# Performance work log

Measured on AMD Instinct MI355X. Metric: run time of the kernel, lower is better.

Reference implementation:

```python
import jax, jax.numpy as jnp
import numpy as np

IMAGE_SIZE = 224          # config.image_size
RP_Q = 10 / 100.0         # config.rp_percentage, 'point' threshold mode
EPS = 1e-8                # normalize_minmax eps
CLIP = 1e-6               # arccos clamp margin


def minmax_global(x):
    """normalize_minmax over the whole tensor (as applied to the raw series)."""
    lo, hi = x.min(), x.max()
    rng = hi - lo
    return jnp.where(rng < EPS, jnp.zeros_like(x), (x - lo) / (rng + EPS))


def minmax_per_matrix(x):
    """normalize_minmax applied independently per (b, d) LxL matrix."""
    lo = x.min(axis=(-2, -1), keepdims=True)
    hi = x.max(axis=(-2, -1), keepdims=True)
    rng = hi - lo
    return jnp.where(rng < EPS, jnp.zeros_like(x), (x - lo) / (rng + EPS))


def setup_inputs() -> dict:
    key = jax.random.key(0)
    x = jax.random.normal(key, (4, 1024, 8), dtype=jnp.float32)  # [B, L, D]
    return {"x": x}


def reference(x):
    B, L, D = x.shape

    # ---- Gramian Angular Field (summation), vectorized over (b, d) ----
    x_norm = minmax_global(x) * 2.0 - 1.0                       # [B, L, D]
    theta = jnp.arccos(jnp.clip(x_norm, -1.0 + CLIP, 1.0 - CLIP))
    th = jnp.transpose(theta, (0, 2, 1))                        # [B, D, L]
    gaf = jnp.cos(th[:, :, :, None] + th[:, :, None, :])        # [B, D, L, L]
    gaf = minmax_per_matrix(gaf)

    # ---- Recurrence plot ('point' quantile threshold), vectorized ----
    s = jnp.transpose(x, (0, 2, 1))                             # [B, D, L]
    dist = jnp.abs(s[:, :, :, None] - s[:, :, None, :])         # [B, D, L, L]
    thr = jnp.quantile(dist.reshape(B, D, L * L), RP_Q, axis=-1)
    rp = (dist <= thr[:, :, None, None]).astype(x.dtype)        # [B, D, L, L]

    # ---- Bilinear resize to (image_size, image_size), align_corners=False ----
    out = jnp.concatenate([gaf, rp], axis=1)                    # [B, 2D, L, L]
    out = jax.image.resize(out, (B, 2 * D, IMAGE_SIZE, IMAGE_SIZE),
                           method="bilinear", antialias=False)
    return out
```

## Files before the change

### kernel.cpp

```cpp
#include <hip/hip_runtime.h>
#include <cfloat>
#include <math.h>

#define B_ 4
#define L_ 1024
#define D_ 8
#define OUT_ 224
#define NPIX (B_ * 2 * D_ * OUT_ * OUT_)
#define NT4  (NPIX / 4)
#define TBL 128
#define TSTR 896

#define NPLANE 32
#define PB 16
#define NBLK (NPLANE * PB)
#define NBIN 2048
#define SLOTCAP 1024
#define GCAP 8192
#define R1U 51917u
#define R2U 51918u

#define SC_PHIST 0u
#define SC_PGAF  ((unsigned)NBLK * (unsigned)NBIN)
#define SC_CNT   (SC_PGAF + (unsigned)NBLK * 2u)
#define SC_BRK   (SC_CNT + (unsigned)NBLK)
#define SC_SLOT  (SC_BRK + (unsigned)NPLANE * 4u)

__device__ __forceinline__ float clipnorm(float v, float lo, float inv2, int degen) {
    float xn = degen ? -1.0f : ((v - lo) * inv2 - 1.0f);
    return fminf(fmaxf(xn, -1.0f + 1e-6f), 1.0f - 1e-6f);
}

__device__ __forceinline__ float sort64(float val, int tid) {
#pragma unroll
    for (int k = 2; k <= 64; k <<= 1) {
        bool up = ((tid & k) == 0);
#pragma unroll
        for (int j = k >> 1; j > 0; j >>= 1) {
            float o = __shfl_xor(val, j);
            bool lower = ((tid & j) == 0);
            float mn = fminf(val, o), mx = fmaxf(val, o);
            val = (lower == up) ? mn : mx;
        }
    }
    return val;
}

__global__ __launch_bounds__(1024) void k_minmax(const float* __restrict__ x,
                                                 float* __restrict__ ws) {
    __shared__ float red[32];
    const int tid  = threadIdx.x;
    const int lane = tid & 63;
    const int wave = tid >> 6;

    float lo = FLT_MAX, hi = -FLT_MAX;
    const float4* x4 = (const float4*)x;
    for (int i = tid; i < (B_ * L_ * D_) / 4; i += 1024) {
        float4 q = x4[i];
        lo = fminf(fminf(fminf(lo, q.x), q.y), fminf(q.z, q.w));
        hi = fmaxf(fmaxf(fmaxf(hi, q.x), q.y), fmaxf(q.z, q.w));
    }
#pragma unroll
    for (int off = 32; off; off >>= 1) {
        lo = fminf(lo, __shfl_down(lo, off));
        hi = fmaxf(hi, __shfl_down(hi, off));
    }
    if (lane == 0) { red[wave] = lo; red[16 + wave] = hi; }
    __syncthreads();
    if (wave == 0 && lane < 16) {
        float l2 = red[lane], h2 = red[16 + lane];
#pragma unroll
        for (int off = 8; off; off >>= 1) {
            l2 = fminf(l2, __shfl_down(l2, off));
            h2 = fmaxf(h2, __shfl_down(h2, off));
        }
        if (lane == 0) { ws[0] = l2; ws[1] = h2; }
    }
}

__global__ __launch_bounds__(256) void k_pairs(const float* __restrict__ x,
                                               const float* __restrict__ ws,
                                               float* __restrict__ wsw,
                                               unsigned* __restrict__ scratch) {
    __shared__ __align__(16) float4 S4[L_];
    __shared__ unsigned hist[NBIN];
    __shared__ float red[16];

    const int tid  = threadIdx.x;
    const int lane = tid & 63;
    const int wave = tid >> 6;
    const int bid  = blockIdx.x;
    const int p    = bid >> 4;
    const int bip  = bid & 15;
    const int b    = p >> 3, d = p & 7;

    const float glo = ws[0], ghi = ws[1];
    const float rng   = ghi - glo;
    const int   degen = rng < 1e-8f;
    const float inv2  = 2.0f / (rng + 1e-8f);
    const float scale = (float)(NBIN - 1) / fmaxf(rng, 1e-20f);

    for (int i = tid; i < L_; i += 256) {
        float v = x[(b * L_ + i) * D_ + d];
        float c = clipnorm(v, glo, inv2, degen);
        S4[i] = make_float4(v, c, sqrtf(fmaxf(0.0f, 1.0f - c * c)), 0.0f);
    }
    for (int i = tid; i < NBIN; i += 256) hist[i] = 0u;
    __syncthreads();

    float4 col[4];
#pragma unroll
    for (int q = 0; q < 4; q++) col[q] = S4[tid + q * 256];

    float gmn = FLT_MAX, gmx = -FLT_MAX;
#pragma unroll
    for (int q = 0; q < 4; q++) {
        float g = col[q].y * col[q].y - col[q].z * col[q].z;
        gmn = fminf(gmn, g); gmx = fmaxf(gmx, g);
    }

    const int obase = bip * 32;
    for (int oo = 1; oo <= 32; ++oo) {
        const int o = obase + oo;
        const int nq = (o == 512) ? 2 : 4;
#pragma unroll
        for (int q = 0; q < 4; q++) {
            if (q < nq) {
                int jp = (tid + q * 256 + o) & 1023;
                float4 P = S4[jp];
                float dd = fabsf(col[q].x - P.x);
                int bin = min((int)(dd * scale), NBIN - 1);
                atomicAdd(&hist[bin], 1u);
                float g = col[q].y * P.y - col[q].z * P.z;
                gmn = fminf(gmn, g); gmx = fmaxf(gmx, g);
            }
        }
    }
    __syncthreads();

    {
        unsigned* ph = scratch + SC_PHIST + (unsigned)bid * NBIN;
        for (int i = tid; i < NBIN; i += 256) ph[i] = hist[i];
    }
#pragma unroll
    for (int off = 32; off; off >>= 1) {
        gmn = fminf(gmn, __shfl_down(gmn, off));
        gmx = fmaxf(gmx, __shfl_down(gmx, off));
    }
    if (lane == 0) { red[wave] = gmn; red[8 + wave] = gmx; }
    __syncthreads();
    if (tid == 0) {
        float* pg = (float*)scratch + SC_PGAF + bid * 2;
        pg[0] = fminf(fminf(red[0], red[1]), fminf(red[2], red[3]));
        pg[1] = fmaxf(fmaxf(red[8], red[9]), fmaxf(red[10], red[11]));
    }
    if (bip == 0) {
        const float scL = (float)L_ / (float)OUT_;
        float* basep = wsw + TBL + p * TSTR;
        for (int o = tid; o < OUT_; o += 256) {
            float fx = (o + 0.5f) * scL - 0.5f;
            int x0 = (int)fx; float wx = fx - (float)x0;
            float q0 = x[(b * L_ + x0) * D_ + d];
            float q1 = x[(b * L_ + x0 + 1) * D_ + d];
            float c0 = clipnorm(q0, glo, inv2, degen), c1 = clipnorm(q1, glo, inv2, degen);
            float s0 = sqrtf(fmaxf(0.0f, 1.0f - c0 * c0)), s1 = sqrtf(fmaxf(0.0f, 1.0f - c1 * c1));
            basep[o]        = c0 + wx * (c1 - c0);
            basep[OUT_ + o] = s0 + wx * (s1 - s0);
            basep[448 + o]  = q0;
            basep[672 + o]  = q1;
        }
    }
}

__global__ __launch_bounds__(256) void k_bracket(float* __restrict__ ws,
                                                 unsigned* __restrict__ scratch) {
    __shared__ unsigned wsum[4];
    __shared__ unsigned sB1, sB2, sBase;

    const int tid  = threadIdx.x;
    const int lane = tid & 63;
    const int wave = tid >> 6;
    const int p    = blockIdx.x;

    unsigned loc[8];
#pragma unroll
    for (int q = 0; q < 8; q++) loc[q] = 0u;
    const unsigned* ph = scratch + SC_PHIST + (unsigned)(p * PB) * NBIN;
    for (int k = 0; k < PB; k++) {
        const uint4* ph4 = (const uint4*)(ph + (unsigned)k * NBIN) + tid * 2;
        uint4 a = ph4[0], c4 = ph4[1];
        loc[0] += a.x; loc[1] += a.y; loc[2] += a.z; loc[3] += a.w;
        loc[4] += c4.x; loc[5] += c4.y; loc[6] += c4.z; loc[7] += c4.w;
    }
    unsigned tsum = 0u;
#pragma unroll
    for (int q = 0; q < 8; q++) tsum += loc[q];
    unsigned inc = tsum;
#pragma unroll
    for (int off = 1; off < 64; off <<= 1) {
        unsigned o = __shfl_up(inc, off);
        if (lane >= off) inc += o;
    }
    if (lane == 63) wsum[wave] = inc;
    __syncthreads();
    unsigned woff = 0u;
    for (int w2 = 0; w2 < 4; w2++) woff += (w2 < wave) ? wsum[w2] : 0u;
    unsigned run = woff + inc - tsum;
#pragma unroll
    for (int q = 0; q < 8; q++) {
        unsigned prev = run; run += loc[q];
        if (prev < R1U && run >= R1U) { sB1 = (unsigned)(tid * 8 + q); sBase = prev; }
        if (prev < R2U && run >= R2U) { sB2 = (unsigned)(tid * 8 + q); }
    }
    __syncthreads();
    if (tid == 0) {
        unsigned* brk = scratch + SC_BRK + (unsigned)p * 4u;
        brk[0] = sB1; brk[1] = sB2; brk[2] = sBase;
    }
    if (tid < 16) {
        const float* pg = (const float*)scratch + SC_PGAF + (unsigned)(p * PB + tid) * 2u;
        float mn = pg[0], mx = pg[1];
#pragma unroll
        for (int off = 8; off; off >>= 1) {
            mn = fminf(mn, __shfl_down(mn, off));
            mx = fmaxf(mx, __shfl_down(mx, off));
        }
        if (tid == 0) {
            ws[2 + p * 3 + 0] = mn;
            ws[2 + p * 3 + 1] = mx;
        }
    }
}

__global__ __launch_bounds__(256) void k_collect(const float* __restrict__ x,
                                                 const float* __restrict__ ws,
                                                 unsigned* __restrict__ scratch) {
    __shared__ float s[L_];
    __shared__ float stage[SLOTCAP];
    __shared__ unsigned scnt;

    const int tid  = threadIdx.x;
    const int bid  = blockIdx.x;
    const int p    = bid >> 4;
    const int bip  = bid & 15;
    const int b    = p >> 3, d = p & 7;

    const float glo = ws[0], ghi = ws[1];
    const float scale = (float)(NBIN - 1) / fmaxf(ghi - glo, 1e-20f);

    const unsigned* brk = scratch + SC_BRK + (unsigned)p * 4u;
    const unsigned B1 = brk[0], B2 = brk[1];
    const float fB1   = (float)B1;
    const float fB2p1 = (B2 >= (unsigned)(NBIN - 1)) ? FLT_MAX : (float)(B2 + 1u);

    for (int i = tid; i < L_; i += 256) s[i] = x[(b * L_ + i) * D_ + d];
    if (tid == 0) scnt = 0u;
    __syncthreads();

    float sj[4];
#pragma unroll
    for (int q = 0; q < 4; q++) sj[q] = s[tid + q * 256];

    const int obase = bip * 32;
    for (int oo = 1; oo <= 32; ++oo) {
        const int o = obase + oo;
        const int nq = (o == 512) ? 2 : 4;
#pragma unroll
        for (int q = 0; q < 4; q++) {
            if (q < nq) {
                int jp = (tid + q * 256 + o) & 1023;
                float dd = fabsf(sj[q] - s[jp]);
                float y = dd * scale;
                if (y >= fB1 && y < fB2p1) {
                    unsigned idx = atomicAdd(&scnt, 1u);
                    if (idx < (unsigned)SLOTCAP) stage[idx] = dd;
                }
            }
        }
    }
    __syncthreads();
    {
        unsigned bc = scnt; bc = (bc < (unsigned)SLOTCAP) ? bc : (unsigned)SLOTCAP;
        float* slot = (float*)scratch + SC_SLOT + (unsigned)bid * SLOTCAP;
        for (unsigned idx = tid; idx < bc; idx += 256) slot[idx] = stage[idx];
        if (tid == 0) scratch[SC_CNT + bid] = bc;
    }
}

__global__ __launch_bounds__(256) void k_select(float* __restrict__ ws,
                                                const unsigned* __restrict__ scratch) {
    __shared__ float cand[GCAP];
    __shared__ float nbuf[2048];
    __shared__ unsigned h2[1024];
    __shared__ unsigned wsum[4];
    __shared__ unsigned scnt, sT1, sT2, sC1, sH1, uminb, umaxb;
    __shared__ float sv1, sv2;
    __shared__ unsigned cpre[17];

    const int tid  = threadIdx.x;
    const int lane = tid & 63;
    const int wave = tid >> 6;
    const int p    = blockIdx.x;

    const float glo = ws[0], ghi = ws[1];
    const float scale = (float)(NBIN - 1) / fmaxf(ghi - glo, 1e-20f);

    const unsigned* brk = scratch + SC_BRK + (unsigned)p * 4u;
    const unsigned B1 = brk[0], B2 = brk[1], base = brk[2];

    if (wave == 0) {
        unsigned c = (lane < PB) ? scratch[SC_CNT + (unsigned)(p * PB + lane)] : 0u;
        unsigned incc = c;
#pragma unroll
        for (int off = 1; off < 16; off <<= 1) {
            unsigned o = __shfl_up(incc, off);
            if ((lane & 15) >= off) incc += o;
        }
        if (lane < PB) { cpre[lane] = incc - c; if (lane == PB - 1) cpre[16] = incc; }
    }
    __syncthreads();

    unsigned n = cpre[16]; n = (n < (unsigned)GCAP) ? n : (unsigned)GCAP;
    for (int k = 0; k < PB; k++) {
        unsigned off = cpre[k];
        unsigned ck  = ((k + 1 < PB) ? cpre[k + 1] : cpre[16]) - cpre[k];
        const float* slot = (const float*)scratch + SC_SLOT + (unsigned)(p * PB + k) * SLOTCAP;
        for (unsigned idx = tid; idx < ck; idx += 256) {
            unsigned dst = off + idx;
            if (dst < (unsigned)GCAP) cand[dst] = slot[idx];
        }
    }
    __syncthreads();

    float* cur = cand;
    float* nxt = nbuf;
    unsigned ncur = n;
    unsigned r1 = R1U - base;
    float vlo = (float)B1 / scale;
    float vhi = (float)(B2 + 1u) / scale;
    float v1 = 0.0f, v2 = 0.0f;
    bool done = false;

    for (int it = 0; it < 6 && !done; ++it) {
        if (tid == 0) scnt = 0u;
#pragma unroll
        for (int q = 0; q < 4; q++) h2[tid + q * 256] = 0u;
        __syncthreads();

        if (ncur <= 64u) {
            if (tid < 64) {
                float val = ((unsigned)tid < ncur) ? cur[tid] : FLT_MAX;
                val = sort64(val, tid);
                float v1l = __shfl(val, (int)r1 - 1);
                float v2l = __shfl(val, (int)r1);
                if (tid == 0) { sv1 = v1l; sv2 = v2l; }
            }
            __syncthreads();
            v1 = sv1; v2 = sv2;
            done = true;
            break;
        }

        float sc2 = 1023.0f / fmaxf(vhi - vlo, 1e-30f);
        for (unsigned k = tid; k < ncur; k += 256) {
            int bb = (int)((cur[k] - vlo) * sc2);
            bb = max(0, min(bb, 1023));
            atomicAdd(&h2[bb], 1u);
        }
        __syncthreads();

        unsigned l[4];
#pragma unroll
        for (int q = 0; q < 4; q++) l[q] = h2[4 * tid + q];
        unsigned tsum = l[0] + l[1] + l[2] + l[3];
        unsigned inc = tsum;
#pragma unroll
        for (int off = 1; off < 64; off <<= 1) {
            unsigned o = __shfl_up(inc, off);
            if (lane >= off) inc += o;
        }
        if (lane == 63) wsum[wave] = inc;
        __syncthreads();
        unsigned woff = 0u;
        for (int w2 = 0; w2 < 4; w2++) woff += (w2 < wave) ? wsum[w2] : 0u;
        unsigned prev = woff + inc - tsum;
#pragma unroll
        for (int q = 0; q < 4; q++) {
            unsigned nrun = prev + l[q];
            if (prev < r1 && nrun >= r1) { sT1 = 4u * tid + q; sC1 = prev; sH1 = l[q]; }
            if (prev < r1 + 1u && nrun >= r1 + 1u) { sT2 = 4u * tid + q; }
            prev = nrun;
        }
        __syncthreads();
        const unsigned t1 = sT1, t2 = sT2, c1 = sC1, h1 = sH1;

        if (t1 != t2) {
            if (tid == 0) { uminb = 0xFFFFFFFFu; umaxb = 0u; }
            __syncthreads();
            for (unsigned k = tid; k < ncur; k += 256) {
                float val = cur[k];
                int bb = (int)((val - vlo) * sc2);
                bb = max(0, min(bb, 1023));
                if (bb == (int)t1) atomicMax(&umaxb, __float_as_uint(val));
                else if (bb > (int)t1) atomicMin(&uminb, __float_as_uint(val));
            }
            __syncthreads();
            v1 = __uint_as_float(umaxb);
            v2 = __uint_as_float(uminb);
            done = true;
            break;
        }

        if (h1 <= 64u) {
            for (unsigned k = tid; k < ncur; k += 256) {
                float val = cur[k];
                int bb = (int)((val - vlo) * sc2);
                bb = max(0, min(bb, 1023));
                if (bb == (int)t1) {
                    unsigned idx = atomicAdd(&scnt, 1u);
                    if (idx < 64u) nxt[idx] = val;
                }
            }
            __syncthreads();
            unsigned cnt = (scnt < 64u) ? scnt : 64u;
            unsigned rr = r1 - c1;
            if (tid < 64) {
                float val = ((unsigned)tid < cnt) ? nxt[tid] : FLT_MAX;
                val = sort64(val, tid);
                float v1l = __shfl(val, (int)rr - 1);
                float v2l = __shfl(val, (int)rr);
                if (tid == 0) { sv1 = v1l; sv2 = v2l; }
            }
            __syncthreads();
            v1 = sv1; v2 = sv2;
            done = true;
            break;
        }

        for (unsigned k = tid; k < ncur; k += 256) {
            float val = cur[k];
            int bb = (int)((val - vlo) * sc2);
            bb = max(0, min(bb, 1023));
            if (bb == (int)t1) {
                unsigned idx = atomicAdd(&scnt, 1u);
                if (idx < 2048u) nxt[idx] = val;
            }
        }
        __syncthreads();
        ncur = (scnt < 2048u) ? scnt : 2048u;
        r1 = r1 - c1;
        float nvlo = vlo + (float)t1 / sc2;
        float nvhi = vlo + (float)(t1 + 1u) / sc2;
        vlo = nvlo; vhi = nvhi;
        float* tmp = cur; cur = nxt; nxt = tmp;
        __syncthreads();
    }
    if (!done) { v1 = vlo; v2 = vhi; }

    if (tid == 0) ws[2 + p * 3 + 2] = v1 + (v2 - v1) * 0.5f;
}

__global__ __launch_bounds__(256) void k_out(const float* __restrict__ ws,
                                             float4* __restrict__ out4) {
    __shared__ __align__(16) float lds[448];
    __shared__ float sc[3];

    const int tid = threadIdx.x;
    int plane = blockIdx.x / 49;
    int c = plane & 15, b = plane >> 4, d = c & 7;

    const float* tb = ws + TBL + (b * 8 + d) * TSTR + ((c < 8) ? 0 : 448);
    for (int i = tid; i < 448; i += 256) lds[i] = tb[i];
    if (tid == 0) {
        if (c < 8) {
            float mn = ws[2 + (b * 8 + d) * 3 + 0];
            float mx = ws[2 + (b * 8 + d) * 3 + 1];
            float g = mx - mn;
            sc[0] = mn;
            sc[1] = (g < 1e-8f) ? 0.0f : 1.0f / (g + 1e-8f);
            sc[2] = (g < 1e-8f) ? 1.0f : 0.0f;
        } else {
            sc[0] = ws[2 + (b * 8 + d) * 3 + 2];
        }
    }
    __syncthreads();

    int tix = blockIdx.x * 256 + tid;
    int pix0 = tix << 2;
    int ox0 = pix0 % OUT_;
    int oy  = (pix0 / OUT_) % OUT_;

    float4 r;
    if (c < 8) {
        float mn = sc[0], ginv = sc[1];
        bool gdeg = sc[2] != 0.0f;
        float Cr = lds[oy], Sr = lds[OUT_ + oy];
        float4 Cc = *(const float4*)&lds[ox0];
        float4 Sc = *(const float4*)&lds[OUT_ + ox0];
        r.x = gdeg ? 0.0f : ((Cr * Cc.x - Sr * Sc.x) - mn) * ginv;
        r.y = gdeg ? 0.0f : ((Cr * Cc.y - Sr * Sc.y) - mn) * ginv;
        r.z = gdeg ? 0.0f : ((Cr * Cc.z - Sr * Sc.z) - mn) * ginv;
        r.w = gdeg ? 0.0f : ((Cr * Cc.w - Sr * Sc.w) - mn) * ginv;
    } else {
        float thr = sc[0];
        const float scale = (float)L_ / (float)OUT_;
        float fy = (oy + 0.5f) * scale - 0.5f;
        int y0 = (int)fy; float wy = fy - (float)y0;
        float r0 = lds[oy], r1 = lds[OUT_ + oy];
        float4 q0 = *(const float4*)&lds[ox0];
        float4 q1 = *(const float4*)&lds[OUT_ + ox0];
        float qq0[4] = {q0.x, q0.y, q0.z, q0.w};
        float qq1[4] = {q1.x, q1.y, q1.z, q1.w};
        float res[4];
#pragma unroll
        for (int pq = 0; pq < 4; pq++) {
            float fx = (ox0 + pq + 0.5f) * scale - 0.5f;
            int x0i = (int)fx; float wx = fx - (float)x0i;
            float v00 = (fabsf(r0 - qq0[pq]) <= thr) ? 1.0f : 0.0f;
            float v01 = (fabsf(r0 - qq1[pq]) <= thr) ? 1.0f : 0.0f;
            float v10 = (fabsf(r1 - qq0[pq]) <= thr) ? 1.0f : 0.0f;
            float v11 = (fabsf(r1 - qq1[pq]) <= thr) ? 1.0f : 0.0f;
            float top = v00 + wx * (v01 - v00);
            float bot = v10 + wx * (v11 - v10);
            res[pq] = top + wy * (bot - top);
        }
        r = make_float4(res[0], res[1], res[2], res[3]);
    }
    out4[tix] = r;
}

extern "C" void kernel_launch(void* const* d_in, const int* in_sizes, int n_in,
                              void* d_out, int out_size, void* d_ws, size_t ws_size,
                              hipStream_t stream) {
    const float* x = (const float*)d_in[0];
    float* ws = (float*)d_ws;
    unsigned* scratch = (unsigned*)d_out;

    k_minmax<<<1, 1024, 0, stream>>>(x, ws);
    k_pairs<<<NBLK, 256, 0, stream>>>(x, ws, ws, scratch);
    k_bracket<<<NPLANE, 256, 0, stream>>>(ws, scratch);
    k_collect<<<NBLK, 256, 0, stream>>>(x, ws, scratch);
    k_select<<<NPLANE, 256, 0, stream>>>(ws, scratch);
    k_out<<<NT4 / 256, 256, 0, stream>>>(ws, (float4*)d_out);
}
```

Measured before the change: 115.9 us.

## Fold global minmax and bracket search into pair and collect kernels

Removes the separate single-block minmax kernel: every k_pairs block now recomputes the global min/max of x itself, and block 0 writes it to the workspace. Removes the k_bracket kernel: every k_collect block redoes the histogram prefix scan for its plane, and only the first block of each plane writes the bracket and GAF min/max out. Splits the shared histogram into four per-wave copies to cut atomic contention, then sums them on write-out. This saves two launches and their serialization gaps, at the cost of redundant reads of x and the per-plane histograms in every block, plus four times the shared memory for histograms.

```diff
diff --git a/kernel.cpp b/kernel.cpp
--- a/kernel.cpp
+++ b/kernel.cpp
@@ -46,44 +46,11 @@
     return val;
 }
 
-__global__ __launch_bounds__(1024) void k_minmax(const float* __restrict__ x,
-                                                 float* __restrict__ ws) {
-    __shared__ float red[32];
-    const int tid  = threadIdx.x;
-    const int lane = tid & 63;
-    const int wave = tid >> 6;
-
-    float lo = FLT_MAX, hi = -FLT_MAX;
-    const float4* x4 = (const float4*)x;
-    for (int i = tid; i < (B_ * L_ * D_) / 4; i += 1024) {
-        float4 q = x4[i];
-        lo = fminf(fminf(fminf(lo, q.x), q.y), fminf(q.z, q.w));
-        hi = fmaxf(fmaxf(fmaxf(hi, q.x), q.y), fmaxf(q.z, q.w));
-    }
-#pragma unroll
-    for (int off = 32; off; off >>= 1) {
-        lo = fminf(lo, __shfl_down(lo, off));
-        hi = fmaxf(hi, __shfl_down(hi, off));
-    }
-    if (lane == 0) { red[wave] = lo; red[16 + wave] = hi; }
-    __syncthreads();
-    if (wave == 0 && lane < 16) {
-        float l2 = red[lane], h2 = red[16 + lane];
-#pragma unroll
-        for (int off = 8; off; off >>= 1) {
-            l2 = fminf(l2, __shfl_down(l2, off));
-            h2 = fmaxf(h2, __shfl_down(h2, off));
-        }
-        if (lane == 0) { ws[0] = l2; ws[1] = h2; }
-    }
-}
-
 __global__ __launch_bounds__(256) void k_pairs(const float* __restrict__ x,
-                                               const float* __restrict__ ws,
-                                               float* __restrict__ wsw,
+                                               float* __restrict__ ws,
                                                unsigned* __restrict__ scratch) {
     __shared__ __align__(16) float4 S4[L_];
-    __shared__ unsigned hist[NBIN];
+    __shared__ __align__(16) unsigned HIST[4 * NBIN];
     __shared__ float red[16];
 
     const int tid  = threadIdx.x;
@@ -94,18 +61,41 @@
     const int bip  = bid & 15;
     const int b    = p >> 3, d = p & 7;
 
-    const float glo = ws[0], ghi = ws[1];
+    float lo = FLT_MAX, hi = -FLT_MAX;
+    {
+        const float4* x4 = (const float4*)x;
+        for (int i = tid; i < (B_ * L_ * D_) / 4; i += 256) {
+            float4 q = x4[i];
+            lo = fminf(fminf(fminf(lo, q.x), q.y), fminf(q.z, q.w));
+            hi = fmaxf(fmaxf(fmaxf(hi, q.x), q.y), fmaxf(q.z, q.w));
+        }
+#pragma unroll
+        for (int off = 32; off; off >>= 1) {
+            lo = fminf(lo, __shfl_down(lo, off));
+            hi = fmaxf(hi, __shfl_down(hi, off));
+        }
+        if (lane == 0) { red[wave] = lo; red[8 + wave] = hi; }
+    }
+    __syncthreads();
+    const float glo = fminf(fminf(red[0], red[1]), fminf(red[2], red[3]));
+    const float ghi = fmaxf(fmaxf(red[8], red[9]), fmaxf(red[10], red[11]));
     const float rng   = ghi - glo;
     const int   degen = rng < 1e-8f;
     const float inv2  = 2.0f / (rng + 1e-8f);
     const float scale = (float)(NBIN - 1) / fmaxf(rng, 1e-20f);
 
+    if (bid == 0 && tid == 0) { ws[0] = glo; ws[1] = ghi; }
+
     for (int i = tid; i < L_; i += 256) {
         float v = x[(b * L_ + i) * D_ + d];
         float c = clipnorm(v, glo, inv2, degen);
         S4[i] = make_float4(v, c, sqrtf(fmaxf(0.0f, 1.0f - c * c)), 0.0f);
     }
-    for (int i = tid; i < NBIN; i += 256) hist[i] = 0u;
+    {
+        uint4 z = make_uint4(0u, 0u, 0u, 0u);
+        uint4* h4 = (uint4*)HIST;
+        for (int i = tid; i < NBIN; i += 256) h4[i] = z;
+    }
     __syncthreads();
 
     float4 col[4];
@@ -119,6 +109,7 @@
         gmn = fminf(gmn, g); gmx = fmaxf(gmx, g);
     }
 
+    unsigned* hw = HIST + wave * NBIN;
     const int obase = bip * 32;
     for (int oo = 1; oo <= 32; ++oo) {
         const int o = obase + oo;
@@ -130,7 +121,7 @@
                 float4 P = S4[jp];
                 float dd = fabsf(col[q].x - P.x);
                 int bin = min((int)(dd * scale), NBIN - 1);
-                atomicAdd(&hist[bin], 1u);
+                atomicAdd(&hw[bin], 1u);
                 float g = col[q].y * P.y - col[q].z * P.z;
                 gmn = fminf(gmn, g); gmx = fmaxf(gmx, g);
             }
@@ -140,7 +131,8 @@
 
     {
         unsigned* ph = scratch + SC_PHIST + (unsigned)bid * NBIN;
-        for (int i = tid; i < NBIN; i += 256) ph[i] = hist[i];
+        for (int i = tid; i < NBIN; i += 256)
+            ph[i] = HIST[i] + HIST[NBIN + i] + HIST[2 * NBIN + i] + HIST[3 * NBIN + i];
     }
 #pragma unroll
     for (int off = 32; off; off >>= 1) {
@@ -156,7 +148,7 @@
     }
     if (bip == 0) {
         const float scL = (float)L_ / (float)OUT_;
-        float* basep = wsw + TBL + p * TSTR;
+        float* basep = ws + TBL + p * TSTR;
         for (int o = tid; o < OUT_; o += 256) {
             float fx = (o + 0.5f) * scL - 0.5f;
             int x0 = (int)fx; float wx = fx - (float)x0;
@@ -172,74 +164,17 @@
     }
 }
 
-__global__ __launch_bounds__(256) void k_bracket(float* __restrict__ ws,
+__global__ __launch_bounds__(256) void k_collect(const float* __restrict__ x,
+                                                 float* __restrict__ ws,
                                                  unsigned* __restrict__ scratch) {
+    __shared__ float s[L_];
+    __shared__ float stage[SLOTCAP];
     __shared__ unsigned wsum[4];
-    __shared__ unsigned sB1, sB2, sBase;
+    __shared__ unsigned sB1, sB2, sBase, scnt;
 
     const int tid  = threadIdx.x;
     const int lane = tid & 63;
     const int wave = tid >> 6;
-    const int p    = blockIdx.x;
-
-    unsigned loc[8];
-#pragma unroll
-    for (int q = 0; q < 8; q++) loc[q] = 0u;
-    const unsigned* ph = scratch + SC_PHIST + (unsigned)(p * PB) * NBIN;
-    for (int k = 0; k < PB; k++) {
-        const uint4* ph4 = (const uint4*)(ph + (unsigned)k * NBIN) + tid * 2;
-        uint4 a = ph4[0], c4 = ph4[1];
-        loc[0] += a.x; loc[1] += a.y; loc[2] += a.z; loc[3] += a.w;
-        loc[4] += c4.x; loc[5] += c4.y; loc[6] += c4.z; loc[7] += c4.w;
-    }
-    unsigned tsum = 0u;
-#pragma unroll
-    for (int q = 0; q < 8; q++) tsum += loc[q];
-    unsigned inc = tsum;
-#pragma unroll
-    for (int off = 1; off < 64; off <<= 1) {
-        unsigned o = __shfl_up(inc, off);
-        if (lane >= off) inc += o;
-    }
-    if (lane == 63) wsum[wave] = inc;
-    __syncthreads();
-    unsigned woff = 0u;
-    for (int w2 = 0; w2 < 4; w2++) woff += (w2 < wave) ? wsum[w2] : 0u;
-    unsigned run = woff + inc - tsum;
-#pragma unroll
-    for (int q = 0; q < 8; q++) {
-        unsigned prev = run; run += loc[q];
-        if (prev < R1U && run >= R1U) { sB1 = (unsigned)(tid * 8 + q); sBase = prev; }
-        if (prev < R2U && run >= R2U) { sB2 = (unsigned)(tid * 8 + q); }
-    }
-    __syncthreads();
-    if (tid == 0) {
-        unsigned* brk = scratch + SC_BRK + (unsigned)p * 4u;
-        brk[0] = sB1; brk[1] = sB2; brk[2] = sBase;
-    }
-    if (tid < 16) {
-        const float* pg = (const float*)scratch + SC_PGAF + (unsigned)(p * PB + tid) * 2u;
-        float mn = pg[0], mx = pg[1];
-#pragma unroll
-        for (int off = 8; off; off >>= 1) {
-            mn = fminf(mn, __shfl_down(mn, off));
-            mx = fmaxf(mx, __shfl_down(mx, off));
-        }
-        if (tid == 0) {
-            ws[2 + p * 3 + 0] = mn;
-            ws[2 + p * 3 + 1] = mx;
-        }
-    }
-}
-
-__global__ __launch_bounds__(256) void k_collect(const float* __restrict__ x,
-                                                 const float* __restrict__ ws,
-                                                 unsigned* __restrict__ scratch) {
-    __shared__ float s[L_];
-    __shared__ float stage[SLOTCAP];
-    __shared__ unsigned scnt;
-
-    const int tid  = threadIdx.x;
     const int bid  = blockIdx.x;
     const int p    = bid >> 4;
     const int bip  = bid & 15;
@@ -248,14 +183,62 @@
     const float glo = ws[0], ghi = ws[1];
     const float scale = (float)(NBIN - 1) / fmaxf(ghi - glo, 1e-20f);
 
-    const unsigned* brk = scratch + SC_BRK + (unsigned)p * 4u;
-    const unsigned B1 = brk[0], B2 = brk[1];
+    for (int i = tid; i < L_; i += 256) s[i] = x[(b * L_ + i) * D_ + d];
+    if (tid == 0) scnt = 0u;
+
+    {
+        unsigned loc[8];
+#pragma unroll
+        for (int q = 0; q < 8; q++) loc[q] = 0u;
+        const unsigned* ph = scratch + SC_PHIST + (unsigned)(p * PB) * NBIN;
+        for (int k = 0; k < PB; k++) {
+            const uint4* ph4 = (const uint4*)(ph + (unsigned)k * NBIN) + tid * 2;
+            uint4 a = ph4[0], c4 = ph4[1];
+            loc[0] += a.x; loc[1] += a.y; loc[2] += a.z; loc[3] += a.w;
+            loc[4] += c4.x; loc[5] += c4.y; loc[6] += c4.z; loc[7] += c4.w;
+        }
+        unsigned tsum = 0u;
+#pragma unroll
+        for (int q = 0; q < 8; q++) tsum += loc[q];
+        unsigned inc = tsum;
+#pragma unroll
+        for (int off = 1; off < 64; off <<= 1) {
+            unsigned o = __shfl_up(inc, off);
+            if (lane >= off) inc += o;
+        }
+        if (lane == 63) wsum[wave] = inc;
+        __syncthreads();
+        unsigned woff = 0u;
+        for (int w2 = 0; w2 < 4; w2++) woff += (w2 < wave) ? wsum[w2] : 0u;
+        unsigned run = woff + inc - tsum;
+#pragma unroll
+        for (int q = 0; q < 8; q++) {
+            unsigned prev = run; run += loc[q];
+            if (prev < R1U && run >= R1U) { sB1 = (unsigned)(tid * 8 + q); sBase = prev; }
+            if (prev < R2U && run >= R2U) { sB2 = (unsigned)(tid * 8 + q); }
+        }
+    }
+    __syncthreads();
+    const unsigned B1 = sB1, B2 = sB2;
+    if (bip == 0 && tid == 0) {
+        unsigned* brk = scratch + SC_BRK + (unsigned)p * 4u;
+        brk[0] = B1; brk[1] = B2; brk[2] = sBase;
+    }
+    if (bip == 0 && tid < 16) {
+        const float* pg = (const float*)scratch + SC_PGAF + (unsigned)(p * PB + tid) * 2u;
+        float mn = pg[0], mx = pg[1];
+#pragma unroll
+        for (int off = 8; off; off >>= 1) {
+            mn = fminf(mn, __shfl_down(mn, off));
+            mx = fmaxf(mx, __shfl_down(mx, off));
+        }
+        if (tid == 0) {
+            ws[2 + p * 3 + 0] = mn;
+            ws[2 + p * 3 + 1] = mx;
+        }
+    }
     const float fB1   = (float)B1;
     const float fB2p1 = (B2 >= (unsigned)(NBIN - 1)) ? FLT_MAX : (float)(B2 + 1u);
-
-    for (int i = tid; i < L_; i += 256) s[i] = x[(b * L_ + i) * D_ + d];
-    if (tid == 0) scnt = 0u;
-    __syncthreads();
 
     float sj[4];
 #pragma unroll
@@ -536,9 +519,7 @@
     float* ws = (float*)d_ws;
     unsigned* scratch = (unsigned*)d_out;
 
-    k_minmax<<<1, 1024, 0, stream>>>(x, ws);
-    k_pairs<<<NBLK, 256, 0, stream>>>(x, ws, ws, scratch);
-    k_bracket<<<NPLANE, 256, 0, stream>>>(ws, scratch);
+    k_pairs<<<NBLK, 256, 0, stream>>>(x, ws, scratch);
     k_collect<<<NBLK, 256, 0, stream>>>(x, ws, scratch);
     k_select<<<NPLANE, 256, 0, stream>>>(ws, scratch);
     k_out<<<NT4 / 256, 256, 0, stream>>>(ws, (float4*)d_out);
```

After: 122.2 us. 1.05x slower.
